# Optimization experiments

Measured on AMD Instinct MI355X. Metric: run time of the kernel, lower is better.

Reference implementation:

```python
import jax, jax.numpy as jnp
import numpy as np

MARGIN = 0.5
EPS = 1e-8  # torch CosineSimilarity eps


def setup_inputs() -> dict:
    key = jax.random.key(0)
    k1, k2 = jax.random.split(key)
    line_end_embeddings = jax.random.normal(k1, (4096, 32, 256), dtype=jnp.float32)
    rhyme_scheme = jax.random.randint(k2, (4096, 32), 0, 4, dtype=jnp.int32)
    return {"line_end_embeddings": line_end_embeddings, "rhyme_scheme": rhyme_scheme}


def reference(line_end_embeddings, rhyme_scheme):
    b, n, d = line_end_embeddings.shape
    # cosine similarity with torch-style eps clamping on norms
    norms = jnp.maximum(jnp.linalg.norm(line_end_embeddings, axis=-1, keepdims=True), EPS)
    unit = line_end_embeddings / norms                       # [b, n, d]
    sims = jnp.einsum("bid,bjd->bij", unit, unit)            # [b, n, n]
    same = rhyme_scheme[:, :, None] == rhyme_scheme[:, None, :]  # [b, n, n]
    per_pair = jnp.where(same, 1.0 - sims, jax.nn.relu(sims - MARGIN))
    # only pairs i < j (strict upper triangle)
    upper = jnp.triu(jnp.ones((n, n), dtype=bool), k=1)
    total = jnp.sum(per_pair * upper[None, :, :])
    count = b * (n * (n - 1) // 2)
    return total / max(count, 1)
```

## Files before the change

kernel.cpp:

```cpp
#include <hip/hip_runtime.h>
#include <hip/hip_bf16.h>
#include <stdint.h>


typedef short bf16x8 __attribute__((ext_vector_type(8)));
typedef float f32x4  __attribute__((ext_vector_type(4)));

#define MARGIN 0.5f
#define EPS_NORM 1e-8f
#define NPAIR_INV (1.0f / 2031616.0f)
#define ROW_STRIDE 260

typedef const __attribute__((address_space(1))) void GVOID;
typedef __attribute__((address_space(3))) void LVOID;

static __device__ __forceinline__ short f2bf(float f) {
    unsigned u = __float_as_uint(f);
    u += 0x7fffu + ((u >> 16) & 1u);
    return (short)(u >> 16);
}

__global__ __launch_bounds__(64) void rhyme_loss_kernel(
    const float* __restrict__ emb,
    const int*   __restrict__ sch,
    float*       __restrict__ out)
{
    __shared__ float s_rows[32 * ROW_STRIDE];
    __shared__ float s_inv[32];
    __shared__ float s_diag[32];
    __shared__ int   s_sch[32];

    const int lane = threadIdx.x;
    const int b    = blockIdx.x;

    const int q = lane >> 4;
    const int c = lane & 15;

    const float* gbase = emb + (size_t)b * 8192 + (size_t)lane * 4;
    #pragma unroll
    for (int r = 0; r < 32; ++r) {
        __builtin_amdgcn_global_load_lds(
            (GVOID*)(gbase + r * 256),
            (LVOID*)(&s_rows[r * ROW_STRIDE]),
            16, 0, 0);
    }

    int mysch = (lane < 32) ? sch[(size_t)b * 32 + lane] : 0;

    __builtin_amdgcn_s_waitcnt(0x0f70);
    __syncthreads();

    if (lane < 32) s_sch[lane] = mysch;

    const float* r0 = s_rows + (size_t)c * ROW_STRIDE + q * 8;
    const float* r1 = s_rows + (size_t)(16 + c) * ROW_STRIDE + q * 8;

    f32x4 acc00 = {0.f, 0.f, 0.f, 0.f};
    f32x4 acc01 = {0.f, 0.f, 0.f, 0.f};
    f32x4 acc11 = {0.f, 0.f, 0.f, 0.f};

    #pragma unroll
    for (int kc = 0; kc < 256; kc += 32) {
        const float4* p0 = (const float4*)(r0 + kc);
        const float4* p1 = (const float4*)(r1 + kc);
        float4 a0 = p0[0], a1 = p0[1];
        float4 b0 = p1[0], b1 = p1[1];

        bf16x8 f0, f1;
        f0[0] = f2bf(a0.x); f0[1] = f2bf(a0.y); f0[2] = f2bf(a0.z); f0[3] = f2bf(a0.w);
        f0[4] = f2bf(a1.x); f0[5] = f2bf(a1.y); f0[6] = f2bf(a1.z); f0[7] = f2bf(a1.w);
        f1[0] = f2bf(b0.x); f1[1] = f2bf(b0.y); f1[2] = f2bf(b0.z); f1[3] = f2bf(b0.w);
        f1[4] = f2bf(b1.x); f1[5] = f2bf(b1.y); f1[6] = f2bf(b1.z); f1[7] = f2bf(b1.w);

        acc00 = __builtin_amdgcn_mfma_f32_16x16x32_bf16(f0, f0, acc00, 0, 0, 0);
        acc01 = __builtin_amdgcn_mfma_f32_16x16x32_bf16(f0, f1, acc01, 0, 0, 0);
        acc11 = __builtin_amdgcn_mfma_f32_16x16x32_bf16(f1, f1, acc11, 0, 0, 0);
    }

    const int dreg = c - 4 * q;
    if (dreg >= 0 && dreg < 4) {
        s_diag[c]      = acc00[dreg];
        s_diag[16 + c] = acc11[dreg];
    }
    __syncthreads();

    if (lane < 32) {
        float d = s_diag[lane];
        s_inv[lane] = 1.0f / fmaxf(sqrtf(d), EPS_NORM);
    }
    __syncthreads();

    const float invj0 = s_inv[c];
    const float invj1 = s_inv[16 + c];
    const int   sj0   = s_sch[c];
    const int   sj1   = s_sch[16 + c];

    float sum = 0.0f;
    #pragma unroll
    for (int r = 0; r < 4; ++r) {
        const int   i0    = q * 4 + r;
        const float inv_i = s_inv[i0];
        const int   si    = s_sch[i0];

        {
            float sim = acc01[r] * inv_i * invj1;
            sum += (si == sj1) ? (1.0f - sim) : fmaxf(sim - MARGIN, 0.0f);
        }
        if (i0 < c) {
            float sim = acc00[r] * inv_i * invj0;
            sum += (si == sj0) ? (1.0f - sim) : fmaxf(sim - MARGIN, 0.0f);
            float sim2 = acc11[r] * s_inv[16 + i0] * invj1;
            sum += (s_sch[16 + i0] == sj1) ? (1.0f - sim2)
                                           : fmaxf(sim2 - MARGIN, 0.0f);
        }
    }

    #pragma unroll
    for (int off = 32; off > 0; off >>= 1)
        sum += __shfl_down(sum, off, 64);

    if (lane == 0)
        atomicAdd(out, sum * NPAIR_INV);
}

extern "C" void kernel_launch(void* const* d_in, const int* in_sizes, int n_in,
                              void* d_out, int out_size, void* d_ws, size_t ws_size,
                              hipStream_t stream) {
    const float* emb = (const float*)d_in[0];
    const int*   sch = (const int*)d_in[1];
    float*       out = (float*)d_out;

    hipMemsetAsync(out, 0, sizeof(float), stream);
    rhyme_loss_kernel<<<dim3(4096), dim3(64), 0, stream>>>(emb, sch, out);
}
```

Measured before the change: 212.0 us.

## Split K dimension across four waves and load directly from global

Uses 256-thread blocks where each wave computes partial Gram-matrix MFMAs over a quarter of the embedding dimension, reading directly from global memory instead of staging rows through LDS. Partial accumulators are reduced through a small shared buffer by wave 0, which then computes norms and the loss. This aims to raise memory-level parallelism and occupancy for a latency-bound load phase, at the cost of an extra LDS reduction and idle waves during the epilogue.

```diff
diff --git a/kernel.cpp b/kernel.cpp
--- a/kernel.cpp
+++ b/kernel.cpp
@@ -9,10 +9,6 @@
 #define MARGIN 0.5f
 #define EPS_NORM 1e-8f
 #define NPAIR_INV (1.0f / 2031616.0f)
-#define ROW_STRIDE 260
-
-typedef const __attribute__((address_space(1))) void GVOID;
-typedef __attribute__((address_space(3))) void LVOID;
 
 static __device__ __forceinline__ short f2bf(float f) {
     unsigned u = __float_as_uint(f);
@@ -20,51 +16,40 @@
     return (short)(u >> 16);
 }
 
-__global__ __launch_bounds__(64) void rhyme_loss_kernel(
+__global__ __launch_bounds__(256, 8) void rhyme_loss_kernel(
     const float* __restrict__ emb,
     const int*   __restrict__ sch,
     float*       __restrict__ out)
 {
-    __shared__ float s_rows[32 * ROW_STRIDE];
+    __shared__ f32x4 s_acc[3][3][64];
+    __shared__ float s_diag[32];
     __shared__ float s_inv[32];
-    __shared__ float s_diag[32];
     __shared__ int   s_sch[32];
 
-    const int lane = threadIdx.x;
+    const int t    = threadIdx.x;
+    const int wv   = t >> 6;
+    const int lane = t & 63;
     const int b    = blockIdx.x;
 
     const int q = lane >> 4;
     const int c = lane & 15;
 
-    const float* gbase = emb + (size_t)b * 8192 + (size_t)lane * 4;
-    #pragma unroll
-    for (int r = 0; r < 32; ++r) {
-        __builtin_amdgcn_global_load_lds(
-            (GVOID*)(gbase + r * 256),
-            (LVOID*)(&s_rows[r * ROW_STRIDE]),
-            16, 0, 0);
-    }
+    if (t < 32)
+        s_sch[t] = sch[(size_t)b * 32 + t];
 
-    int mysch = (lane < 32) ? sch[(size_t)b * 32 + lane] : 0;
-
-    __builtin_amdgcn_s_waitcnt(0x0f70);
-    __syncthreads();
-
-    if (lane < 32) s_sch[lane] = mysch;
-
-    const float* r0 = s_rows + (size_t)c * ROW_STRIDE + q * 8;
-    const float* r1 = s_rows + (size_t)(16 + c) * ROW_STRIDE + q * 8;
+    const float* base0 = emb + (size_t)b * 8192 + (size_t)c * 256 + wv * 64 + q * 8;
+    const float* base1 = base0 + 16 * 256;
 
     f32x4 acc00 = {0.f, 0.f, 0.f, 0.f};
     f32x4 acc01 = {0.f, 0.f, 0.f, 0.f};
     f32x4 acc11 = {0.f, 0.f, 0.f, 0.f};
 
     #pragma unroll
-    for (int kc = 0; kc < 256; kc += 32) {
-        const float4* p0 = (const float4*)(r0 + kc);
-        const float4* p1 = (const float4*)(r1 + kc);
-        float4 a0 = p0[0], a1 = p0[1];
-        float4 b0 = p1[0], b1 = p1[1];
+    for (int kc = 0; kc < 64; kc += 32) {
+        float4 a0 = *(const float4*)(base0 + kc);
+        float4 a1 = *(const float4*)(base0 + kc + 4);
+        float4 b0 = *(const float4*)(base1 + kc);
+        float4 b1 = *(const float4*)(base1 + kc + 4);
 
         bf16x8 f0, f1;
         f0[0] = f2bf(a0.x); f0[1] = f2bf(a0.y); f0[2] = f2bf(a0.z); f0[3] = f2bf(a0.w);
@@ -77,50 +62,63 @@
         acc11 = __builtin_amdgcn_mfma_f32_16x16x32_bf16(f1, f1, acc11, 0, 0, 0);
     }
 
-    const int dreg = c - 4 * q;
-    if (dreg >= 0 && dreg < 4) {
-        s_diag[c]      = acc00[dreg];
-        s_diag[16 + c] = acc11[dreg];
+    if (wv != 0) {
+        s_acc[wv - 1][0][lane] = acc00;
+        s_acc[wv - 1][1][lane] = acc01;
+        s_acc[wv - 1][2][lane] = acc11;
     }
     __syncthreads();
 
-    if (lane < 32) {
-        float d = s_diag[lane];
-        s_inv[lane] = 1.0f / fmaxf(sqrtf(d), EPS_NORM);
+    if (wv == 0) {
+        #pragma unroll
+        for (int p = 0; p < 3; ++p) {
+            acc00 += s_acc[p][0][lane];
+            acc01 += s_acc[p][1][lane];
+            acc11 += s_acc[p][2][lane];
+        }
+
+        const int dreg = c - 4 * q;
+        if (dreg >= 0 && dreg < 4) {
+            s_diag[c]      = acc00[dreg];
+            s_diag[16 + c] = acc11[dreg];
+        }
+        __builtin_amdgcn_wave_barrier();
+        if (lane < 32)
+            s_inv[lane] = 1.0f / fmaxf(sqrtf(s_diag[lane]), EPS_NORM);
+        __builtin_amdgcn_wave_barrier();
+
+        const float invj0 = s_inv[c];
+        const float invj1 = s_inv[16 + c];
+        const int   sj0   = s_sch[c];
+        const int   sj1   = s_sch[16 + c];
+
+        float sum = 0.0f;
+        #pragma unroll
+        for (int r = 0; r < 4; ++r) {
+            const int   i0    = q * 4 + r;
+            const float inv_i = s_inv[i0];
+            const int   si    = s_sch[i0];
+
+            {
+                float sim = acc01[r] * inv_i * invj1;
+                sum += (si == sj1) ? (1.0f - sim) : fmaxf(sim - MARGIN, 0.0f);
+            }
+            if (i0 < c) {
+                float sim = acc00[r] * inv_i * invj0;
+                sum += (si == sj0) ? (1.0f - sim) : fmaxf(sim - MARGIN, 0.0f);
+                float sim2 = acc11[r] * s_inv[16 + i0] * invj1;
+                sum += (s_sch[16 + i0] == sj1) ? (1.0f - sim2)
+                                               : fmaxf(sim2 - MARGIN, 0.0f);
+            }
+        }
+
+        #pragma unroll
+        for (int off = 32; off > 0; off >>= 1)
+            sum += __shfl_down(sum, off, 64);
+
+        if (lane == 0)
+            atomicAdd(out, sum * NPAIR_INV);
     }
-    __syncthreads();
-
-    const float invj0 = s_inv[c];
-    const float invj1 = s_inv[16 + c];
-    const int   sj0   = s_sch[c];
-    const int   sj1   = s_sch[16 + c];
-
-    float sum = 0.0f;
-    #pragma unroll
-    for (int r = 0; r < 4; ++r) {
-        const int   i0    = q * 4 + r;
-        const float inv_i = s_inv[i0];
-        const int   si    = s_sch[i0];
-
-        {
-            float sim = acc01[r] * inv_i * invj1;
-            sum += (si == sj1) ? (1.0f - sim) : fmaxf(sim - MARGIN, 0.0f);
-        }
-        if (i0 < c) {
-            float sim = acc00[r] * inv_i * invj0;
-            sum += (si == sj0) ? (1.0f - sim) : fmaxf(sim - MARGIN, 0.0f);
-            float sim2 = acc11[r] * s_inv[16 + i0] * invj1;
-            sum += (s_sch[16 + i0] == sj1) ? (1.0f - sim2)
-                                           : fmaxf(sim2 - MARGIN, 0.0f);
-        }
-    }
-
-    #pragma unroll
-    for (int off = 32; off > 0; off >>= 1)
-        sum += __shfl_down(sum, off, 64);
-
-    if (lane == 0)
-        atomicAdd(out, sum * NPAIR_INV);
 }
 
 extern "C" void kernel_launch(void* const* d_in, const int* in_sizes, int n_in,
@@ -131,5 +129,5 @@
     float*       out = (float*)d_out;
 
     hipMemsetAsync(out, 0, sizeof(float), stream);
-    rhyme_loss_kernel<<<dim3(4096), dim3(64), 0, stream>>>(emb, sch, out);
+    rhyme_loss_kernel<<<dim3(4096), dim3(256), 0, stream>>>(emb, sch, out);
 }
```

Result: faster. 206.9 us (-2.4%).
